# Kernel tuning notes

Hardware: AMD Instinct MI355X
Metric: run time of the kernel (lower is better)

## Reference

```python
import jax, jax.numpy as jnp
import numpy as np

# Vehicle / drivetrain constants (match init_kwargs and hard-coded source constants)
LF, LR = 1.5, 1.4
CM1, CM2 = 550.0, 650.0
MASS, IZ = 1265.0, 2000.0
DT = 0.01
C_DRIVE = 3.45 * 0.919 / (0.34 * 1265.0)  # gear-ratio constant from source
GRAV = 9.8


def _mlp(a, w1, b1, w2, b2):
    # 1 -> 12 -> 1 MLP applied per-row. a: [B]; w1,b1,w2: [12]; b2: scalar
    h = jax.nn.relu(a[:, None] * w1[None, :] + b1[None, :])  # [B, 12]
    return h @ w2 + b2  # [B]


def setup_inputs() -> dict:
    key = jax.random.key(0)
    ks = jax.random.split(key, 7)
    B = 4_194_304
    x = jax.random.normal(ks[0], (B, 8), dtype=jnp.float32)
    # First-layer init as in source: weight filled with 1.0, bias = arange(-0.6, 0.6, 0.1)
    b1 = (-0.6 + 0.1 * jnp.arange(12)).astype(jnp.float32)
    bound = float(1.0 / np.sqrt(12.0))  # torch default init bound for Linear(12, 1)
    return {
        "x": x,
        "fy_w1": jnp.ones((12,), jnp.float32),
        "fy_b1": b1,
        "fy_w2": jax.random.uniform(ks[1], (12,), jnp.float32, -bound, bound),
        "fy_b2": jax.random.uniform(ks[2], (), jnp.float32, -bound, bound),
        "ry_w1": jnp.ones((12,), jnp.float32),
        "ry_b1": b1,
        "ry_w2": jax.random.uniform(ks[3], (12,), jnp.float32, -bound, bound),
        "ry_b2": jax.random.uniform(ks[4], (), jnp.float32, -bound, bound),
        "rx_w": jax.random.uniform(ks[5], (), jnp.float32, -1.0, 1.0),
        "rx_b": jax.random.uniform(ks[6], (), jnp.float32, -1.0, 1.0),
    }


def reference(x, fy_w1, fy_b1, fy_w2, fy_b2, ry_w1, ry_b1, ry_w2, ry_b2, rx_w, rx_b):
    pwm = x[:, 0]
    theta = x[:, 2]
    pitch = x[:, 7]
    out = jnp.zeros_like(x[:, 3:6])  # [B, 3] accumulated (dvx, dvy, dw)

    def fy(a):
        return _mlp(a, fy_w1, fy_b1, fy_w2, fy_b2)

    def ry(a):
        return _mlp(a, ry_w1, ry_b1, ry_w2, ry_b2)

    st, ct = jnp.sin(theta), jnp.cos(theta)
    sp = jnp.sin(pitch)
    a_pred = jnp.where(pwm > 0.0, CM1, CM2) * pwm * C_DRIVE

    for _ in range(2):  # fixed 2-step integration loop, as in source
        vx = x[:, 3] + out[:, 0]
        vy = x[:, 4] + out[:, 1]
        w = x[:, 5] + out[:, 2]
        alpha_f = theta - jnp.arctan2(w * LF + vy, vx)
        alpha_r = jnp.arctan2(w * LR - vy, vx)
        # Fy(a)*(a>0) - Fy(-a)*(a<=0): exactly one branch survives per element
        Ffy = jnp.where(alpha_f > 0.0, fy(alpha_f), -fy(-alpha_f))
        Fry = jnp.where(alpha_r > 0.0, ry(alpha_r), -ry(-alpha_r))
        Frx = a_pred + rx_w * vx * vx + rx_b  # Rx(vx^2) + drivetrain accel
        vx_dot = Frx - Ffy * st + vy * w - GRAV * sp
        vy_dot = Fry + Ffy * ct - vx * w
        w_dot = MASS * (Ffy * LF * ct - Fry * LR) / IZ
        out = out + DT * jnp.stack([vx_dot, vy_dot, w_dot], axis=1)
    return out
```

## Files before the change

kernel.cpp:

```cpp
#include <hip/hip_runtime.h>
#include <math.h>

#define DEV_INLINE __device__ __forceinline__

DEV_INLINE float fast_atan2f(float y, float x) {
    const float kPI  = 3.14159265358979323846f;
    const float kPI2 = 1.57079632679489661923f;
    float ax = fabsf(x), ay = fabsf(y);
    float mx = fmaxf(ax, ay);
    float mn = fminf(ax, ay);
    float a  = mn * __builtin_amdgcn_rcpf(mx);
    float s  = a * a;
    float p  = -0.01172120f;
    p = fmaf(p, s,  0.05265332f);
    p = fmaf(p, s, -0.11643287f);
    p = fmaf(p, s,  0.19354346f);
    p = fmaf(p, s, -0.33262347f);
    p = fmaf(p, s,  0.99997726f);
    float r = a * p;
    r = (ay > ax)   ? (kPI2 - r) : r;
    r = (x < 0.0f)  ? (kPI  - r) : r;
    return copysignf(r, y);
}

DEV_INLINE float mlp12(float a, const float* __restrict__ w1,
                       const float* __restrict__ b1,
                       const float* __restrict__ w2, float b2) {
    float acc = b2;
#pragma unroll
    for (int j = 0; j < 12; ++j) {
        float h = fmaxf(fmaf(a, w1[j], b1[j]), 0.0f);
        acc = fmaf(h, w2[j], acc);
    }
    return acc;
}

__global__ __launch_bounds__(256) void dyn_kernel(
    const float4* __restrict__ x4,
    const float* __restrict__ fy_w1, const float* __restrict__ fy_b1,
    const float* __restrict__ fy_w2, const float* __restrict__ fy_b2,
    const float* __restrict__ ry_w1, const float* __restrict__ ry_b1,
    const float* __restrict__ ry_w2, const float* __restrict__ ry_b2,
    const float* __restrict__ rx_w, const float* __restrict__ rx_b,
    float* __restrict__ out, int nrows) {
    const float kLF     = 1.5f;
    const float kLR     = 1.4f;
    const float kCM1    = 550.0f;
    const float kCM2    = 650.0f;
    const float kDT     = 0.01f;
    const float kGRAV   = 9.8f;
    const float kCDRIVE = (float)(3.45 * 0.919 / (0.34 * 1265.0));
    const float kWF     = (float)(1265.0 * 1.5 / 2000.0);
    const float kWR     = (float)(1265.0 * 1.4 / 2000.0);

    __shared__ float sout[768];

    float fw1[12], fb1[12], fw2[12];
    float rw1[12], rb1[12], rw2[12];
#pragma unroll
    for (int j = 0; j < 12; ++j) {
        fw1[j] = fy_w1[j]; fb1[j] = fy_b1[j]; fw2[j] = fy_w2[j];
        rw1[j] = ry_w1[j]; rb1[j] = ry_b1[j]; rw2[j] = ry_w2[j];
    }
    const float fb2 = fy_b2[0];
    const float rb2 = ry_b2[0];
    const float rxw = rx_w[0];
    const float rxb = rx_b[0];

    const int tid = threadIdx.x;
    const long long t = (long long)blockIdx.x * 256 + tid;

    float o0 = 0.0f, o1 = 0.0f, o2 = 0.0f;
    if (t < nrows) {
        const float4 lo = x4[2 * t];
        const float4 hi = x4[2 * t + 1];

        const float pwm   = lo.x;
        const float theta = lo.z;
        const float x3    = lo.w;
        const float x4v   = hi.x;
        const float x5    = hi.y;
        const float pitch = hi.w;

        const float st = __sinf(theta);
        const float ct = __cosf(theta);
        const float sp = __sinf(pitch);
        const float a_pred = (pwm > 0.0f ? kCM1 : kCM2) * pwm * kCDRIVE;

#pragma unroll
        for (int it = 0; it < 2; ++it) {
            const float vx = x3 + o0;
            const float vy = x4v + o1;
            const float w  = x5 + o2;

            const float af = theta - fast_atan2f(fmaf(w, kLF, vy), vx);
            const float ar = fast_atan2f(fmaf(w, kLR, -vy), vx);

            const float sf  = af > 0.0f ? 1.0f : -1.0f;
            const float Ffy = sf * mlp12(sf * af, fw1, fb1, fw2, fb2);
            const float sr  = ar > 0.0f ? 1.0f : -1.0f;
            const float Fry = sr * mlp12(sr * ar, rw1, rb1, rw2, rb2);

            const float Frx = fmaf(rxw * vx, vx, a_pred + rxb);

            const float vx_dot = Frx - Ffy * st + vy * w - kGRAV * sp;
            const float vy_dot = Fry + Ffy * ct - vx * w;
            const float w_dot  = kWF * Ffy * ct - kWR * Fry;

            o0 = fmaf(kDT, vx_dot, o0);
            o1 = fmaf(kDT, vy_dot, o1);
            o2 = fmaf(kDT, w_dot,  o2);
        }
    }

    sout[tid * 3 + 0] = o0;
    sout[tid * 3 + 1] = o1;
    sout[tid * 3 + 2] = o2;
    __syncthreads();

    const long long gbase = (long long)blockIdx.x * 768;
    const long long gmax  = (long long)nrows * 3;
#pragma unroll
    for (int j = 0; j < 3; ++j) {
        const long long gi = gbase + j * 256 + tid;
        if (gi < gmax) out[gi] = sout[j * 256 + tid];
    }
}

extern "C" void kernel_launch(void* const* d_in, const int* in_sizes, int n_in,
                              void* d_out, int out_size, void* d_ws, size_t ws_size,
                              hipStream_t stream) {
    const float4* x4   = (const float4*)d_in[0];
    const float* fy_w1 = (const float*)d_in[1];
    const float* fy_b1 = (const float*)d_in[2];
    const float* fy_w2 = (const float*)d_in[3];
    const float* fy_b2 = (const float*)d_in[4];
    const float* ry_w1 = (const float*)d_in[5];
    const float* ry_b1 = (const float*)d_in[6];
    const float* ry_w2 = (const float*)d_in[7];
    const float* ry_b2 = (const float*)d_in[8];
    const float* rx_w  = (const float*)d_in[9];
    const float* rx_b  = (const float*)d_in[10];

    const int nrows = in_sizes[0] / 8;
    const int threads = 256;
    const int blocks = (nrows + threads - 1) / threads;

    dyn_kernel<<<blocks, threads, 0, stream>>>(
        x4, fy_w1, fy_b1, fy_w2, fy_b2, ry_w1, ry_b1, ry_w2, ry_b2, rx_w, rx_b,
        (float*)d_out, nrows);
}
```

Baseline: 218.5 us.

## Stage coalesced input loads through LDS and process two rows per thread

Each block now handles 512 rows with 256 threads. The whole input tile is loaded with consecutive-float4 coalesced reads, transposed into shared memory as a column layout, and each thread then computes two rows. This replaces the per-thread strided 32-byte row reads and amortises the per-thread weight-register setup over twice the work. It costs 16KB of LDS per block, which may lower occupancy, adds extra barriers, and the LDS column writes may hit bank conflicts.

```diff
diff --git a/kernel.cpp b/kernel.cpp
--- a/kernel.cpp
+++ b/kernel.cpp
@@ -35,14 +35,13 @@
     return acc;
 }
 
-__global__ __launch_bounds__(256) void dyn_kernel(
-    const float4* __restrict__ x4,
-    const float* __restrict__ fy_w1, const float* __restrict__ fy_b1,
-    const float* __restrict__ fy_w2, const float* __restrict__ fy_b2,
-    const float* __restrict__ ry_w1, const float* __restrict__ ry_b1,
-    const float* __restrict__ ry_w2, const float* __restrict__ ry_b2,
-    const float* __restrict__ rx_w, const float* __restrict__ rx_b,
-    float* __restrict__ out, int nrows) {
+struct Row { float pwm, theta, vx0, vy0, w0, pitch; };
+
+DEV_INLINE void compute_row(const Row& in,
+                            const float* fw1, const float* fb1, const float* fw2, float fb2,
+                            const float* rw1, const float* rb1, const float* rw2, float rb2,
+                            float rxw, float rxb,
+                            float& o0, float& o1, float& o2) {
     const float kLF     = 1.5f;
     const float kLR     = 1.4f;
     const float kCM1    = 550.0f;
@@ -53,7 +52,47 @@
     const float kWF     = (float)(1265.0 * 1.5 / 2000.0);
     const float kWR     = (float)(1265.0 * 1.4 / 2000.0);
 
-    __shared__ float sout[768];
+    const float st = __sinf(in.theta);
+    const float ct = __cosf(in.theta);
+    const float sp = __sinf(in.pitch);
+    const float a_pred = (in.pwm > 0.0f ? kCM1 : kCM2) * in.pwm * kCDRIVE;
+
+    o0 = 0.0f; o1 = 0.0f; o2 = 0.0f;
+#pragma unroll
+    for (int it = 0; it < 2; ++it) {
+        const float vx = in.vx0 + o0;
+        const float vy = in.vy0 + o1;
+        const float w  = in.w0  + o2;
+
+        const float af = in.theta - fast_atan2f(fmaf(w, kLF, vy), vx);
+        const float ar = fast_atan2f(fmaf(w, kLR, -vy), vx);
+
+        const float sf  = af > 0.0f ? 1.0f : -1.0f;
+        const float Ffy = sf * mlp12(sf * af, fw1, fb1, fw2, fb2);
+        const float sr  = ar > 0.0f ? 1.0f : -1.0f;
+        const float Fry = sr * mlp12(sr * ar, rw1, rb1, rw2, rb2);
+
+        const float Frx = fmaf(rxw * vx, vx, a_pred + rxb);
+
+        const float vx_dot = Frx - Ffy * st + vy * w - kGRAV * sp;
+        const float vy_dot = Fry + Ffy * ct - vx * w;
+        const float w_dot  = kWF * Ffy * ct - kWR * Fry;
+
+        o0 = fmaf(kDT, vx_dot, o0);
+        o1 = fmaf(kDT, vy_dot, o1);
+        o2 = fmaf(kDT, w_dot,  o2);
+    }
+}
+
+__global__ __launch_bounds__(256) void dyn_kernel(
+    const float4* __restrict__ x4,
+    const float* __restrict__ fy_w1, const float* __restrict__ fy_b1,
+    const float* __restrict__ fy_w2, const float* __restrict__ fy_b2,
+    const float* __restrict__ ry_w1, const float* __restrict__ ry_b1,
+    const float* __restrict__ ry_w2, const float* __restrict__ ry_b2,
+    const float* __restrict__ rx_w, const float* __restrict__ rx_b,
+    float* __restrict__ out, int nrows) {
+    __shared__ float sIn[8 * 512];
 
     float fw1[12], fb1[12], fw2[12];
     float rw1[12], rb1[12], rw2[12];
@@ -68,62 +107,57 @@
     const float rxb = rx_b[0];
 
     const int tid = threadIdx.x;
-    const long long t = (long long)blockIdx.x * 256 + tid;
-
-    float o0 = 0.0f, o1 = 0.0f, o2 = 0.0f;
-    if (t < nrows) {
-        const float4 lo = x4[2 * t];
-        const float4 hi = x4[2 * t + 1];
-
-        const float pwm   = lo.x;
-        const float theta = lo.z;
-        const float x3    = lo.w;
-        const float x4v   = hi.x;
-        const float x5    = hi.y;
-        const float pitch = hi.w;
-
-        const float st = __sinf(theta);
-        const float ct = __cosf(theta);
-        const float sp = __sinf(pitch);
-        const float a_pred = (pwm > 0.0f ? kCM1 : kCM2) * pwm * kCDRIVE;
+    const long long rowBase = (long long)blockIdx.x * 512;
+    const long long f4Base  = rowBase * 2;
+    const long long f4Max   = (long long)nrows * 2;
 
 #pragma unroll
-        for (int it = 0; it < 2; ++it) {
-            const float vx = x3 + o0;
-            const float vy = x4v + o1;
-            const float w  = x5 + o2;
-
-            const float af = theta - fast_atan2f(fmaf(w, kLF, vy), vx);
-            const float ar = fast_atan2f(fmaf(w, kLR, -vy), vx);
-
-            const float sf  = af > 0.0f ? 1.0f : -1.0f;
-            const float Ffy = sf * mlp12(sf * af, fw1, fb1, fw2, fb2);
-            const float sr  = ar > 0.0f ? 1.0f : -1.0f;
-            const float Fry = sr * mlp12(sr * ar, rw1, rb1, rw2, rb2);
-
-            const float Frx = fmaf(rxw * vx, vx, a_pred + rxb);
-
-            const float vx_dot = Frx - Ffy * st + vy * w - kGRAV * sp;
-            const float vy_dot = Fry + Ffy * ct - vx * w;
-            const float w_dot  = kWF * Ffy * ct - kWR * Fry;
-
-            o0 = fmaf(kDT, vx_dot, o0);
-            o1 = fmaf(kDT, vy_dot, o1);
-            o2 = fmaf(kDT, w_dot,  o2);
-        }
+    for (int q = 0; q < 4; ++q) {
+        const int l = q * 256 + tid;
+        const long long g = f4Base + l;
+        float4 f = make_float4(0.f, 0.f, 0.f, 0.f);
+        if (g < f4Max) f = x4[g];
+        const int row = l >> 1;
+        const int c0  = (l & 1) * 4;
+        sIn[(c0 + 0) * 512 + row] = f.x;
+        sIn[(c0 + 1) * 512 + row] = f.y;
+        sIn[(c0 + 2) * 512 + row] = f.z;
+        sIn[(c0 + 3) * 512 + row] = f.w;
     }
-
-    sout[tid * 3 + 0] = o0;
-    sout[tid * 3 + 1] = o1;
-    sout[tid * 3 + 2] = o2;
     __syncthreads();
 
-    const long long gbase = (long long)blockIdx.x * 768;
+    float o[2][3];
+#pragma unroll
+    for (int h = 0; h < 2; ++h) {
+        const int r = h * 256 + tid;
+        Row in;
+        in.pwm   = sIn[0 * 512 + r];
+        in.theta = sIn[2 * 512 + r];
+        in.vx0   = sIn[3 * 512 + r];
+        in.vy0   = sIn[4 * 512 + r];
+        in.w0    = sIn[5 * 512 + r];
+        in.pitch = sIn[7 * 512 + r];
+        compute_row(in, fw1, fb1, fw2, fb2, rw1, rb1, rw2, rb2, rxw, rxb,
+                    o[h][0], o[h][1], o[h][2]);
+    }
+    __syncthreads();
+
+    float* sOut = sIn;
+#pragma unroll
+    for (int h = 0; h < 2; ++h) {
+        const int r = h * 256 + tid;
+        sOut[r * 3 + 0] = o[h][0];
+        sOut[r * 3 + 1] = o[h][1];
+        sOut[r * 3 + 2] = o[h][2];
+    }
+    __syncthreads();
+
+    const long long gbase = rowBase * 3;
     const long long gmax  = (long long)nrows * 3;
 #pragma unroll
-    for (int j = 0; j < 3; ++j) {
+    for (int j = 0; j < 6; ++j) {
         const long long gi = gbase + j * 256 + tid;
-        if (gi < gmax) out[gi] = sout[j * 256 + tid];
+        if (gi < gmax) out[gi] = sOut[j * 256 + tid];
     }
 }
 
@@ -143,10 +177,10 @@
     const float* rx_b  = (const float*)d_in[10];
 
     const int nrows = in_sizes[0] / 8;
-    const int threads = 256;
-    const int blocks = (nrows + threads - 1) / threads;
+    const int rows_per_block = 512;
+    const int blocks = (nrows + rows_per_block - 1) / rows_per_block;
 
-    dyn_kernel<<<blocks, threads, 0, stream>>>(
+    dyn_kernel<<<blocks, 256, 0, stream>>>(
         x4, fy_w1, fy_b1, fy_w2, fy_b2, ry_w1, ry_b1, ry_w2, ry_b2, rx_w, rx_b,
         (float*)d_out, nrows);
 }
```

New measurement: 225.1 us. 1.03x slower.
